# Kernel tuning notes

Hardware: AMD Instinct MI355X
Metric: run time of the kernel (lower is better)

Reference implementation:

```python
import jax, jax.numpy as jnp
import numpy as np

NUM_HEADS = 16
MASKED_BIAS = -10000.0


def setup_inputs() -> dict:
    key = jax.random.key(0)
    k1, k2, k3 = jax.random.split(key, 3)
    B, S, D = 2, 2048, 1024
    return {
        "hidden_states": jax.random.normal(k1, (B, S, D), dtype=jnp.float32),
        "c_attn_w": jax.random.normal(k2, (D, 3 * D), dtype=jnp.float32) * 0.02,
        "c_attn_b": jnp.zeros((3 * D,), dtype=jnp.float32),
        "c_proj_w": jax.random.normal(k3, (D, D), dtype=jnp.float32) * 0.02,
        "c_proj_b": jnp.zeros((D,), dtype=jnp.float32),
    }


def reference(hidden_states, c_attn_w, c_attn_b, c_proj_w, c_proj_b):
    B, S, D = hidden_states.shape
    H = NUM_HEADS
    hd = D // H

    qkv = hidden_states @ c_attn_w + c_attn_b  # [B, S, 3D]
    q, k, v = jnp.split(qkv, 3, axis=-1)

    def split_heads(t):
        return t.reshape(B, S, H, hd).transpose(0, 2, 1, 3)  # [B, H, S, hd]

    q, k, v = split_heads(q), split_heads(k), split_heads(v)

    attn_weights = jnp.einsum("bhqd,bhkd->bhqk", q, k)
    attn_weights = attn_weights / jnp.sqrt(jnp.float32(hd))
    # multiplicative causal mask, matching eager GPT2: w*mask + (-1e4)*(1-mask)
    causal = jnp.tril(jnp.ones((S, S), dtype=attn_weights.dtype))  # [S, S]
    attn_weights = attn_weights * causal + MASKED_BIAS * (1.0 - causal)
    attn_weights = jax.nn.softmax(attn_weights, axis=-1)

    attn_output = jnp.einsum("bhqk,bhkd->bhqd", attn_weights, v)
    attn_output = attn_output.transpose(0, 2, 1, 3).reshape(B, S, D)
    attn_output = attn_output @ c_proj_w + c_proj_b
    return attn_output, attn_weights
```

## Files before the change

### kernel.cpp

```cpp
#include <hip/hip_runtime.h>


typedef __bf16 bf16_t;
typedef bf16_t bf16x8 __attribute__((ext_vector_type(8)));
typedef float f32x4 __attribute__((ext_vector_type(4)));
typedef unsigned short ushort8 __attribute__((ext_vector_type(8)));
typedef unsigned short ushort4v __attribute__((ext_vector_type(4)));

#define SEQ 2048
#define DMODEL 1024
#define MTOT 4096

#define AS1 __attribute__((address_space(1)))
#define AS3 __attribute__((address_space(3)))

__device__ __forceinline__ unsigned short f2bf(float f) {
  return __builtin_bit_cast(unsigned short, (bf16_t)f);
}
__device__ __forceinline__ float bf2f(unsigned short u) {
  return __builtin_bit_cast(float, (unsigned)u << 16);
}
__device__ __forceinline__ bf16x8 ldb8(const unsigned short* p) {
  return __builtin_bit_cast(bf16x8, *(const ushort8*)p);
}
__device__ __forceinline__ f32x4 mfma16(bf16x8 a, bf16x8 b, f32x4 c) {
  return __builtin_amdgcn_mfma_f32_16x16x32_bf16(a, b, c, 0, 0, 0);
}
__device__ __forceinline__ void gload16(const unsigned short* g, unsigned short* l) {
  __builtin_amdgcn_global_load_lds((AS1 const void*)g, (AS3 void*)l, 16, 0, 0);
}

__global__ __launch_bounds__(256) void cast_kernel(const float* __restrict__ in,
                                                   unsigned short* __restrict__ out) {
  int i = blockIdx.x * 256 + threadIdx.x;
  float4 v = ((const float4*)in)[i];
  ushort4v o;
  o[0] = f2bf(v.x); o[1] = f2bf(v.y); o[2] = f2bf(v.z); o[3] = f2bf(v.w);
  ((ushort4v*)out)[i] = o;
}

__global__ __launch_bounds__(256) void transpose_cast_kernel(const float* __restrict__ in,
                                                             unsigned short* __restrict__ out,
                                                             int R, int C) {
  __shared__ float tile[32][33];
  int c0 = blockIdx.x * 32, r0 = blockIdx.y * 32;
  int tx = threadIdx.x & 31, ty = threadIdx.x >> 5;
#pragma unroll
  for (int i = 0; i < 4; ++i)
    tile[ty + i * 8][tx] = in[(size_t)(r0 + ty + i * 8) * C + c0 + tx];
  __syncthreads();
#pragma unroll
  for (int i = 0; i < 4; ++i)
    out[(size_t)(c0 + ty + i * 8) * R + r0 + tx] = f2bf(tile[tx][ty + i * 8]);
}

template <int EPI>
__global__ __launch_bounds__(256) void gemm128(
    const unsigned short* __restrict__ A, const unsigned short* __restrict__ BT,
    const float* __restrict__ bias, float* __restrict__ outF,
    unsigned short* __restrict__ qws, unsigned short* __restrict__ kws,
    unsigned short* __restrict__ vws, int M, int N, int K) {
  __shared__ unsigned short Alds[128 * 32];
  __shared__ unsigned short Blds[128 * 32];
  int m0 = blockIdx.x * 128, n0 = blockIdx.y * 128;
  int t = threadIdx.x;
  int l = t & 63, j = l & 15, g = l >> 4;
  int w = t >> 6, wr = w >> 1, wc = w & 1;

  f32x4 acc[4][4];
#pragma unroll
  for (int mi = 0; mi < 4; ++mi)
#pragma unroll
    for (int st = 0; st < 4; ++st)
#pragma unroll
      for (int r = 0; r < 4; ++r) acc[mi][st][r] = 0.f;

  int srow = t >> 2;
  int scol = (t & 3) * 8;
  const unsigned short* aB0 = A + (size_t)(m0 + srow) * K + scol;
  const unsigned short* aB1 = aB0 + (size_t)64 * K;
  const unsigned short* bB0 = BT + (size_t)(n0 + srow) * K + scol;
  const unsigned short* bB1 = bB0 + (size_t)64 * K;
  unsigned short* aL0 = &Alds[srow * 32 + scol];
  unsigned short* aL1 = aL0 + 64 * 32;
  unsigned short* bL0 = &Blds[srow * 32 + scol];
  unsigned short* bL1 = bL0 + 64 * 32;

  for (int k0 = 0; k0 < K; k0 += 32) {
    __syncthreads();
    gload16(aB0 + k0, aL0);
    gload16(aB1 + k0, aL1);
    gload16(bB0 + k0, bL0);
    gload16(bB1 + k0, bL1);
    __syncthreads();
    bf16x8 af[4], bfr[4];
#pragma unroll
    for (int mi = 0; mi < 4; ++mi) af[mi] = ldb8(&Alds[(wr * 64 + mi * 16 + j) * 32 + g * 8]);
#pragma unroll
    for (int st = 0; st < 4; ++st) bfr[st] = ldb8(&Blds[(wc * 64 + st * 16 + j) * 32 + g * 8]);
#pragma unroll
    for (int mi = 0; mi < 4; ++mi)
#pragma unroll
      for (int st = 0; st < 4; ++st) acc[mi][st] = mfma16(af[mi], bfr[st], acc[mi][st]);
  }

#pragma unroll
  for (int st = 0; st < 4; ++st) {
    int n = n0 + wc * 64 + st * 16 + j;
    float bv = bias[n];
#pragma unroll
    for (int mi = 0; mi < 4; ++mi)
#pragma unroll
      for (int r = 0; r < 4; ++r) {
        int m = m0 + wr * 64 + mi * 16 + g * 4 + r;
        float val = acc[mi][st][r] + bv;
        if (EPI == 1) {
          outF[(size_t)m * N + n] = val;
        } else {
          int region = n >> 10;
          int h = (n & 1023) >> 6;
          int d = n & 63;
          int bb = m >> 11, s = m & 2047;
          int bh = bb * 16 + h;
          if (region == 0) qws[(((size_t)bh) * SEQ + s) * 64 + d] = f2bf(val * 0.125f);
          else if (region == 1) kws[(((size_t)bh) * SEQ + s) * 64 + d] = f2bf(val);
          else vws[(((size_t)bh) * 64 + d) * SEQ + s] = f2bf(val);
        }
      }
  }
}

__global__ __launch_bounds__(256) void attn_kernel(
    const unsigned short* __restrict__ qg, const unsigned short* __restrict__ kg,
    const unsigned short* __restrict__ vg, float* __restrict__ outw,
    unsigned short* __restrict__ ointer) {
  __shared__ unsigned short Klds[64 * 64];
  __shared__ unsigned short Vlds[64 * 64];
  __shared__ unsigned short Plds[4][16][72];

  int v = blockIdx.x;
  int qt = (v & 1) ? ((v - 1) >> 1) : (31 - (v >> 1));
  int bh = blockIdx.y;
  int b = bh >> 4, h = bh & 15;
  int t = threadIdx.x;
  int w = t >> 6, l = t & 63, j = l & 15, g = l >> 4;

  const unsigned short* qb = qg + (size_t)bh * SEQ * 64;
  const unsigned short* kb = kg + (size_t)bh * SEQ * 64;
  const unsigned short* vb = vg + (size_t)bh * SEQ * 64;
  float* outrow = outw + (size_t)bh * SEQ * SEQ;

  int qr_a = qt * 64 + w * 16 + j;
  bf16x8 qa0 = ldb8(&qb[(size_t)qr_a * 64 + g * 8]);
  bf16x8 qa1 = ldb8(&qb[(size_t)qr_a * 64 + 32 + g * 8]);

  int qrow0 = qt * 64 + w * 16 + g * 4;

  int srow = t >> 3;
  int swz8 = ((t & 7) ^ (srow & 7)) * 8;
  const unsigned short* ksrc0 = kb + srow * 64 + swz8;
  const unsigned short* ksrc1 = ksrc0 + 32 * 64;
  const unsigned short* vsrc0 = vb + (size_t)srow * SEQ + swz8;
  const unsigned short* vsrc1 = vsrc0 + (size_t)32 * SEQ;
  unsigned short* kd0 = &Klds[t * 8];
  unsigned short* kd1 = kd0 + 2048;
  unsigned short* vd0 = &Vlds[t * 8];
  unsigned short* vd1 = vd0 + 2048;

  int rb0 = j * 64 + ((g ^ (j & 7)) * 8);
  int rb1 = j * 64 + (((4 + g) ^ (j & 7)) * 8);

  float lpart[4] = {0.f, 0.f, 0.f, 0.f};

  for (int kt = 0; kt <= qt; ++kt) {
    __syncthreads();
    gload16(ksrc0 + kt * 4096, kd0);
    gload16(ksrc1 + kt * 4096, kd1);
    __syncthreads();
    f32x4 sacc[4];
#pragma unroll
    for (int st = 0; st < 4; ++st)
#pragma unroll
      for (int r = 0; r < 4; ++r) sacc[st][r] = 0.f;
#pragma unroll
    for (int st = 0; st < 4; ++st) {
      bf16x8 kf0 = ldb8(&Klds[st * 1024 + rb0]);
      bf16x8 kf1 = ldb8(&Klds[st * 1024 + rb1]);
      sacc[st] = mfma16(qa0, kf0, sacc[st]);
      sacc[st] = mfma16(qa1, kf1, sacc[st]);
    }
    bool diag = (kt == qt);
#pragma unroll
    for (int r = 0; r < 4; ++r) {
      int qrow = qrow0 + r;
#pragma unroll
      for (int st = 0; st < 4; ++st) {
        float p = __expf(sacc[st][r]);
        if (diag) {
          int kc = kt * 64 + st * 16 + j;
          p = (kc > qrow) ? 0.f : p;
        }
        lpart[r] += p;
      }
    }
  }

  float linv[4];
#pragma unroll
  for (int r = 0; r < 4; ++r) {
    float sum = lpart[r];
#pragma unroll
    for (int o = 1; o < 16; o <<= 1) sum += __shfl_xor(sum, o);
    linv[r] = 1.f / sum;
  }

  f32x4 oacc[4];
#pragma unroll
  for (int st = 0; st < 4; ++st)
#pragma unroll
    for (int r = 0; r < 4; ++r) oacc[st][r] = 0.f;

  int prow = l >> 2;
  int pch = l & 3;

  for (int kt = 0; kt < SEQ / 64; ++kt) {
    if (kt <= qt) {
      __syncthreads();
      gload16(ksrc0 + kt * 4096, kd0);
      gload16(ksrc1 + kt * 4096, kd1);
      gload16(vsrc0 + kt * 64, vd0);
      gload16(vsrc1 + kt * 64, vd1);
      __syncthreads();
      f32x4 sacc[4];
#pragma unroll
      for (int st = 0; st < 4; ++st)
#pragma unroll
        for (int r = 0; r < 4; ++r) sacc[st][r] = 0.f;
#pragma unroll
      for (int st = 0; st < 4; ++st) {
        bf16x8 kf0 = ldb8(&Klds[st * 1024 + rb0]);
        bf16x8 kf1 = ldb8(&Klds[st * 1024 + rb1]);
        sacc[st] = mfma16(qa0, kf0, sacc[st]);
        sacc[st] = mfma16(qa1, kf1, sacc[st]);
      }
      bool diag = (kt == qt);
#pragma unroll
      for (int st = 0; st < 4; ++st) {
#pragma unroll
        for (int r = 0; r < 4; ++r) {
          int qrow = qrow0 + r;
          int kc = kt * 64 + st * 16 + j;
          float p = __expf(sacc[st][r]) * linv[r];
          if (diag) p = (kc > qrow) ? 0.f : p;
          Plds[w][g * 4 + r][st * 16 + j] = f2bf(p);
        }
      }
#pragma unroll
      for (int it = 0; it < 2; ++it) {
        int ch = pch + it * 4;
        ushort8 pv = *(const ushort8*)&Plds[w][prow][ch * 8];
        float4 f0, f1;
        f0.x = bf2f(pv[0]); f0.y = bf2f(pv[1]); f0.z = bf2f(pv[2]); f0.w = bf2f(pv[3]);
        f1.x = bf2f(pv[4]); f1.y = bf2f(pv[5]); f1.z = bf2f(pv[6]); f1.w = bf2f(pv[7]);
        float* dst = &outrow[(size_t)(qt * 64 + w * 16 + prow) * SEQ + kt * 64 + ch * 8];
        ((float4*)dst)[0] = f0;
        ((float4*)dst)[1] = f1;
      }
      bf16x8 pa0 = ldb8(&Plds[w][j][g * 8]);
      bf16x8 pa1 = ldb8(&Plds[w][j][32 + g * 8]);
#pragma unroll
      for (int st = 0; st < 4; ++st) {
        bf16x8 vf0 = ldb8(&Vlds[st * 1024 + rb0]);
        bf16x8 vf1 = ldb8(&Vlds[st * 1024 + rb1]);
        oacc[st] = mfma16(pa0, vf0, oacc[st]);
        oacc[st] = mfma16(pa1, vf1, oacc[st]);
      }
    } else {
      int row = qt * 64 + w * 16 + (l >> 2);
      int c0 = kt * 64 + (l & 3) * 16;
      float4 z = make_float4(0.f, 0.f, 0.f, 0.f);
      float4* zp = (float4*)&outrow[(size_t)row * SEQ + c0];
      zp[0] = z; zp[1] = z; zp[2] = z; zp[3] = z;
    }
  }

#pragma unroll
  for (int st = 0; st < 4; ++st)
#pragma unroll
    for (int r = 0; r < 4; ++r) {
      int qrow = qrow0 + r;
      int d = st * 16 + j;
      ointer[((size_t)b * SEQ + qrow) * DMODEL + h * 64 + d] = f2bf(oacc[st][r]);
    }
}

extern "C" void kernel_launch(void* const* d_in, const int* in_sizes, int n_in,
                              void* d_out, int out_size, void* d_ws, size_t ws_size,
                              hipStream_t stream) {
  const float* hidden = (const float*)d_in[0];
  const float* w_attn = (const float*)d_in[1];
  const float* b_attn = (const float*)d_in[2];
  const float* w_proj = (const float*)d_in[3];
  const float* b_proj = (const float*)d_in[4];

  float* out_attn = (float*)d_out;
  float* out_w = out_attn + (size_t)MTOT * DMODEL;

  char* ws = (char*)d_ws;
  unsigned short* hbf = (unsigned short*)(ws);
  unsigned short* w1T = (unsigned short*)(ws + 8388608);
  unsigned short* w2T = (unsigned short*)(ws + 14680064);
  unsigned short* qws = (unsigned short*)(ws + 16777216);
  unsigned short* kws = (unsigned short*)(ws + 25165824);
  unsigned short* vws = (unsigned short*)(ws + 33554432);

  cast_kernel<<<4096, 256, 0, stream>>>(hidden, hbf);
  transpose_cast_kernel<<<dim3(96, 32), 256, 0, stream>>>(w_attn, w1T, 1024, 3072);
  transpose_cast_kernel<<<dim3(32, 32), 256, 0, stream>>>(w_proj, w2T, 1024, 1024);
  gemm128<0><<<dim3(32, 24), 256, 0, stream>>>(hbf, w1T, b_attn, nullptr, qws, kws, vws,
                                               MTOT, 3 * DMODEL, DMODEL);
  attn_kernel<<<dim3(32, 32), 256, 0, stream>>>(qws, kws, vws, out_w, hbf);
  gemm128<1><<<dim3(32, 8), 256, 0, stream>>>(hbf, w2T, b_proj, out_attn, nullptr, nullptr,
                                              nullptr, MTOT, DMODEL, DMODEL);
}
```

Baseline: 267.4 us.

## Pair complementary query tiles per 512-thread block to share K/V loads

Each attention block now runs 8 waves covering two query tiles, qt and 31-qt, so every block does the same amount of causal work. Each K/V tile is loaded into LDS once and used by both halves, which roughly halves redundant global K/V traffic. Zeroing of the masked upper triangle moves to after the main loops. The cost is that the waves working on the shorter tile sit idle at barriers while the longer tile finishes, and the block count halves, which may lower occupancy.

```diff
diff --git a/kernel.cpp b/kernel.cpp
--- a/kernel.cpp
+++ b/kernel.cpp
@@ -130,107 +130,51 @@
   }
 }
 
-__global__ __launch_bounds__(256) void attn_kernel(
+__global__ __launch_bounds__(512) void attn_kernel(
     const unsigned short* __restrict__ qg, const unsigned short* __restrict__ kg,
     const unsigned short* __restrict__ vg, float* __restrict__ outw,
     unsigned short* __restrict__ ointer) {
   __shared__ unsigned short Klds[64 * 64];
   __shared__ unsigned short Vlds[64 * 64];
-  __shared__ unsigned short Plds[4][16][72];
-
-  int v = blockIdx.x;
-  int qt = (v & 1) ? ((v - 1) >> 1) : (31 - (v >> 1));
+  __shared__ unsigned short Plds[8][16 * 72];
+
+  int qtA = blockIdx.x;
+  int qtB = 31 - qtA;
   int bh = blockIdx.y;
   int b = bh >> 4, h = bh & 15;
   int t = threadIdx.x;
-  int w = t >> 6, l = t & 63, j = l & 15, g = l >> 4;
+  int wv = t >> 6, l = t & 63, j = l & 15, g = l >> 4;
+  int wl = wv & 3;
+  int qt = (wv >= 4) ? qtB : qtA;
 
   const unsigned short* qb = qg + (size_t)bh * SEQ * 64;
   const unsigned short* kb = kg + (size_t)bh * SEQ * 64;
   const unsigned short* vb = vg + (size_t)bh * SEQ * 64;
   float* outrow = outw + (size_t)bh * SEQ * SEQ;
 
-  int qr_a = qt * 64 + w * 16 + j;
+  int qr_a = qt * 64 + wl * 16 + j;
   bf16x8 qa0 = ldb8(&qb[(size_t)qr_a * 64 + g * 8]);
   bf16x8 qa1 = ldb8(&qb[(size_t)qr_a * 64 + 32 + g * 8]);
 
-  int qrow0 = qt * 64 + w * 16 + g * 4;
+  int qrow0 = qt * 64 + wl * 16 + g * 4;
 
   int srow = t >> 3;
   int swz8 = ((t & 7) ^ (srow & 7)) * 8;
-  const unsigned short* ksrc0 = kb + srow * 64 + swz8;
-  const unsigned short* ksrc1 = ksrc0 + 32 * 64;
-  const unsigned short* vsrc0 = vb + (size_t)srow * SEQ + swz8;
-  const unsigned short* vsrc1 = vsrc0 + (size_t)32 * SEQ;
-  unsigned short* kd0 = &Klds[t * 8];
-  unsigned short* kd1 = kd0 + 2048;
-  unsigned short* vd0 = &Vlds[t * 8];
-  unsigned short* vd1 = vd0 + 2048;
+  const unsigned short* ksrc = kb + srow * 64 + swz8;
+  const unsigned short* vsrc = vb + (size_t)srow * SEQ + swz8;
+  unsigned short* kd = &Klds[t * 8];
+  unsigned short* vd = &Vlds[t * 8];
 
   int rb0 = j * 64 + ((g ^ (j & 7)) * 8);
   int rb1 = j * 64 + (((4 + g) ^ (j & 7)) * 8);
 
   float lpart[4] = {0.f, 0.f, 0.f, 0.f};
 
-  for (int kt = 0; kt <= qt; ++kt) {
-    __syncthreads();
-    gload16(ksrc0 + kt * 4096, kd0);
-    gload16(ksrc1 + kt * 4096, kd1);
-    __syncthreads();
-    f32x4 sacc[4];
-#pragma unroll
-    for (int st = 0; st < 4; ++st)
-#pragma unroll
-      for (int r = 0; r < 4; ++r) sacc[st][r] = 0.f;
-#pragma unroll
-    for (int st = 0; st < 4; ++st) {
-      bf16x8 kf0 = ldb8(&Klds[st * 1024 + rb0]);
-      bf16x8 kf1 = ldb8(&Klds[st * 1024 + rb1]);
-      sacc[st] = mfma16(qa0, kf0, sacc[st]);
-      sacc[st] = mfma16(qa1, kf1, sacc[st]);
-    }
-    bool diag = (kt == qt);
-#pragma unroll
-    for (int r = 0; r < 4; ++r) {
-      int qrow = qrow0 + r;
-#pragma unroll
-      for (int st = 0; st < 4; ++st) {
-        float p = __expf(sacc[st][r]);
-        if (diag) {
-          int kc = kt * 64 + st * 16 + j;
-          p = (kc > qrow) ? 0.f : p;
-        }
-        lpart[r] += p;
-      }
-    }
-  }
-
-  float linv[4];
-#pragma unroll
-  for (int r = 0; r < 4; ++r) {
-    float sum = lpart[r];
-#pragma unroll
-    for (int o = 1; o < 16; o <<= 1) sum += __shfl_xor(sum, o);
-    linv[r] = 1.f / sum;
-  }
-
-  f32x4 oacc[4];
-#pragma unroll
-  for (int st = 0; st < 4; ++st)
-#pragma unroll
-    for (int r = 0; r < 4; ++r) oacc[st][r] = 0.f;
-
-  int prow = l >> 2;
-  int pch = l & 3;
-
-  for (int kt = 0; kt < SEQ / 64; ++kt) {
+  for (int kt = 0; kt <= qtB; ++kt) {
+    __syncthreads();
+    gload16(ksrc + kt * 4096, kd);
+    __syncthreads();
     if (kt <= qt) {
-      __syncthreads();
-      gload16(ksrc0 + kt * 4096, kd0);
-      gload16(ksrc1 + kt * 4096, kd1);
-      gload16(vsrc0 + kt * 64, vd0);
-      gload16(vsrc1 + kt * 64, vd1);
-      __syncthreads();
       f32x4 sacc[4];
 #pragma unroll
       for (int st = 0; st < 4; ++st)
@@ -245,6 +189,59 @@
       }
       bool diag = (kt == qt);
 #pragma unroll
+      for (int r = 0; r < 4; ++r) {
+        int qrow = qrow0 + r;
+#pragma unroll
+        for (int st = 0; st < 4; ++st) {
+          float p = __expf(sacc[st][r]);
+          if (diag) {
+            int kc = kt * 64 + st * 16 + j;
+            p = (kc > qrow) ? 0.f : p;
+          }
+          lpart[r] += p;
+        }
+      }
+    }
+  }
+
+  float linv[4];
+#pragma unroll
+  for (int r = 0; r < 4; ++r) {
+    float sum = lpart[r];
+#pragma unroll
+    for (int o = 1; o < 16; o <<= 1) sum += __shfl_xor(sum, o);
+    linv[r] = 1.f / sum;
+  }
+
+  f32x4 oacc[4];
+#pragma unroll
+  for (int st = 0; st < 4; ++st)
+#pragma unroll
+    for (int r = 0; r < 4; ++r) oacc[st][r] = 0.f;
+
+  int prow = l >> 2;
+  int pch = l & 3;
+
+  for (int kt = 0; kt <= qtB; ++kt) {
+    __syncthreads();
+    gload16(ksrc + kt * 4096, kd);
+    gload16(vsrc + kt * 64, vd);
+    __syncthreads();
+    if (kt <= qt) {
+      f32x4 sacc[4];
+#pragma unroll
+      for (int st = 0; st < 4; ++st)
+#pragma unroll
+        for (int r = 0; r < 4; ++r) sacc[st][r] = 0.f;
+#pragma unroll
+      for (int st = 0; st < 4; ++st) {
+        bf16x8 kf0 = ldb8(&Klds[st * 1024 + rb0]);
+        bf16x8 kf1 = ldb8(&Klds[st * 1024 + rb1]);
+        sacc[st] = mfma16(qa0, kf0, sacc[st]);
+        sacc[st] = mfma16(qa1, kf1, sacc[st]);
+      }
+      bool diag = (kt == qt);
+#pragma unroll
       for (int st = 0; st < 4; ++st) {
 #pragma unroll
         for (int r = 0; r < 4; ++r) {
@@ -252,22 +249,22 @@
           int kc = kt * 64 + st * 16 + j;
           float p = __expf(sacc[st][r]) * linv[r];
           if (diag) p = (kc > qrow) ? 0.f : p;
-          Plds[w][g * 4 + r][st * 16 + j] = f2bf(p);
+          Plds[wv][(g * 4 + r) * 72 + st * 16 + j] = f2bf(p);
         }
       }
 #pragma unroll
       for (int it = 0; it < 2; ++it) {
         int ch = pch + it * 4;
-        ushort8 pv = *(const ushort8*)&Plds[w][prow][ch * 8];
+        ushort8 pv = *(const ushort8*)&Plds[wv][prow * 72 + ch * 8];
         float4 f0, f1;
         f0.x = bf2f(pv[0]); f0.y = bf2f(pv[1]); f0.z = bf2f(pv[2]); f0.w = bf2f(pv[3]);
         f1.x = bf2f(pv[4]); f1.y = bf2f(pv[5]); f1.z = bf2f(pv[6]); f1.w = bf2f(pv[7]);
-        float* dst = &outrow[(size_t)(qt * 64 + w * 16 + prow) * SEQ + kt * 64 + ch * 8];
+        float* dst = &outrow[(size_t)(qt * 64 + wl * 16 + prow) * SEQ + kt * 64 + ch * 8];
         ((float4*)dst)[0] = f0;
         ((float4*)dst)[1] = f1;
       }
-      bf16x8 pa0 = ldb8(&Plds[w][j][g * 8]);
-      bf16x8 pa1 = ldb8(&Plds[w][j][32 + g * 8]);
+      bf16x8 pa0 = ldb8(&Plds[wv][j * 72 + g * 8]);
+      bf16x8 pa1 = ldb8(&Plds[wv][j * 72 + 32 + g * 8]);
 #pragma unroll
       for (int st = 0; st < 4; ++st) {
         bf16x8 vf0 = ldb8(&Vlds[st * 1024 + rb0]);
@@ -275,12 +272,6 @@
         oacc[st] = mfma16(pa0, vf0, oacc[st]);
         oacc[st] = mfma16(pa1, vf1, oacc[st]);
       }
-    } else {
-      int row = qt * 64 + w * 16 + (l >> 2);
-      int c0 = kt * 64 + (l & 3) * 16;
-      float4 z = make_float4(0.f, 0.f, 0.f, 0.f);
-      float4* zp = (float4*)&outrow[(size_t)row * SEQ + c0];
-      zp[0] = z; zp[1] = z; zp[2] = z; zp[3] = z;
     }
   }
 
@@ -292,6 +283,16 @@
       int d = st * 16 + j;
       ointer[((size_t)b * SEQ + qrow) * DMODEL + h * 64 + d] = f2bf(oacc[st][r]);
     }
+
+  {
+    int row = qt * 64 + wl * 16 + (l >> 2);
+    int cc = (l & 3) * 16;
+    float4 z = make_float4(0.f, 0.f, 0.f, 0.f);
+    for (int kt = qt + 1; kt < SEQ / 64; ++kt) {
+      float4* zp = (float4*)&outrow[(size_t)row * SEQ + kt * 64 + cc];
+      zp[0] = z; zp[1] = z; zp[2] = z; zp[3] = z;
+    }
+  }
 }
 
 extern "C" void kernel_launch(void* const* d_in, const int* in_sizes, int n_in,
@@ -319,7 +320,7 @@
   transpose_cast_kernel<<<dim3(32, 32), 256, 0, stream>>>(w_proj, w2T, 1024, 1024);
   gemm128<0><<<dim3(32, 24), 256, 0, stream>>>(hbf, w1T, b_attn, nullptr, qws, kws, vws,
                                                MTOT, 3 * DMODEL, DMODEL);
-  attn_kernel<<<dim3(32, 32), 256, 0, stream>>>(qws, kws, vws, out_w, hbf);
+  attn_kernel<<<dim3(16, 32), 512, 0, stream>>>(qws, kws, vws, out_w, hbf);
   gemm128<1><<<dim3(32, 8), 256, 0, stream>>>(hbf, w2T, b_proj, out_attn, nullptr, nullptr,
                                               nullptr, MTOT, DMODEL, DMODEL);
 }
```

Measured after the change: 462.7 us. +73.0%, slower.
